# Optimization experiments

Hardware: AMD Instinct MI355X
Metric: run time of the kernel (lower is better)

Reference implementation:

```python
import jax, jax.numpy as jnp
import numpy as np

DIM = 384
HEADS = 12
HEAD_DIM = DIM // HEADS
WIN = (2, 7, 7)
NW_TOK = WIN[0] * WIN[1] * WIN[2]  # 98
SCALE = HEAD_DIM ** -0.5


def _relative_position_index():
    d = np.arange(WIN[0]); h = np.arange(WIN[1]); w = np.arange(WIN[2])
    coords = np.stack(np.meshgrid(d, h, w, indexing='ij'))  # [3,D,H,W]
    cf = coords.reshape(3, -1)  # [3, NW_TOK]
    rel = cf[:, :, None] - cf[:, None, :]  # [3, N, N]
    rel = rel.transpose(1, 2, 0).astype(np.int64)
    rel[:, :, 0] += WIN[0] - 1
    rel[:, :, 1] += WIN[1] - 1
    rel[:, :, 2] += WIN[2] - 1
    rel[:, :, 0] *= (2 * WIN[1] - 1) * (2 * WIN[2] - 1)
    rel[:, :, 1] *= 2 * WIN[2] - 1
    return rel.sum(-1)  # [NW_TOK, NW_TOK]


def setup_inputs() -> dict:
    key = jax.random.key(0)
    ks = jax.random.split(key, 6)
    B_, N = 1024, NW_TOK + 1
    nW = 64
    table_len = (2 * WIN[0] - 1) * (2 * WIN[1] - 1) * (2 * WIN[2] - 1)  # 507
    x = jax.random.normal(ks[0], (B_, N, DIM), dtype=jnp.float32)
    mask = jax.random.normal(ks[1], (nW, NW_TOK, NW_TOK), dtype=jnp.float32)
    W_qkv = jax.random.normal(ks[2], (DIM, 3 * DIM), dtype=jnp.float32) * 0.02
    rpb_table = jax.random.normal(ks[3], (table_len, HEADS), dtype=jnp.float32) * 0.02
    W_proj = jax.random.normal(ks[4], (DIM, DIM), dtype=jnp.float32) * 0.02
    b_proj = jnp.zeros((DIM,), dtype=jnp.float32)
    rpi = jnp.asarray(_relative_position_index(), dtype=jnp.int32)
    return {"x": x, "mask": mask, "W_qkv": W_qkv, "rpb_table": rpb_table,
            "W_proj": W_proj, "b_proj": b_proj, "rpi": rpi}


def reference(x, mask, W_qkv, rpb_table, W_proj, b_proj, rpi):
    B_, N, C = x.shape
    qkv = (x @ W_qkv).reshape(B_, N, 3, HEADS, HEAD_DIM)
    q, k, v = qkv[:, :, 0], qkv[:, :, 1], qkv[:, :, 2]  # [B_, N, H, hd]
    attn = jnp.einsum('bnhd,bmhd->bhnm', q * SCALE, k)  # [B_, H, N, N]
    # gathered relative position bias over non-class tokens, zero-padded for class token
    bias = rpb_table[rpi.reshape(-1)].reshape(NW_TOK, NW_TOK, HEADS).transpose(2, 0, 1)
    bias_full = jnp.pad(bias, ((0, 0), (1, 0), (1, 0)))  # [H, N, N]
    attn = attn + bias_full[None]
    nW = mask.shape[0]
    mask_full = jnp.pad(mask, ((0, 0), (1, 0), (1, 0)))  # [nW, N, N]
    attn = attn.reshape(B_ // nW, nW, HEADS, N, N) + mask_full[None, :, None]
    attn = attn.reshape(B_, HEADS, N, N)
    attn = jax.nn.softmax(attn, axis=-1)
    out = jnp.einsum('bhnm,bmhd->bnhd', attn, v).reshape(B_, N, C)
    out = out @ W_proj + b_proj
    return out[:, 1:], out[:, :1]
```

## Files before the change

### kernel.cpp

```cpp
#include <hip/hip_runtime.h>
#include <hip/hip_bf16.h>
#include <cstddef>
#include <cstdint>


using bf16 = __hip_bfloat16;
typedef short v8s __attribute__((ext_vector_type(8)));
typedef float v4f __attribute__((ext_vector_type(4)));

static constexpr int    NTOK   = 99;
static constexpr int    CDIM   = 384;
static constexpr int    NHEAD  = 12;
static constexpr int    NROWS  = 101376;
static constexpr size_t PLANE  = (size_t)NROWS * 32;
static constexpr float  SCALEF = 0.17677669529663687f;

__device__ __forceinline__ v4f mfma16x16x32(v8s a, v8s b, v4f c) {
  return __builtin_amdgcn_mfma_f32_16x16x32_bf16(a, b, c, 0, 0, 0);
}
__device__ __forceinline__ short f2bf(float f) {
  bf16 h = __float2bfloat16(f);
  return *reinterpret_cast<short*>(&h);
}

static constexpr size_t WT_QKV_OFF = 0;
static constexpr size_t WT_P_OFF   = 884736;
static constexpr size_t BIAS_OFF   = 884736 + 294912;
static constexpr size_t COMMON_END = 1650096;
static constexpr size_t O_WS_OFF   = COMMON_END;
static constexpr size_t WS_MID     = O_WS_OFF + (size_t)NROWS * 384 * 2;
static constexpr size_t BM_OFF     = COMMON_END;
static constexpr size_t QKV_OFF    = BM_OFF + (size_t)64 * NHEAD * NTOK * NTOK * 4;
static constexpr size_t WS_FULL    = QKV_OFF + (size_t)NROWS * 1152 * 2;

static constexpr int PREP_BASE = 1152 * 384 + 384 * 384 + NHEAD * 99 * 99;
static constexpr int PREP_BM   = 64 * NHEAD * 99 * 99;

__global__ void prep_kernel(const float* __restrict__ Wqkv, const float* __restrict__ Wproj,
                            const float* __restrict__ rpb,  const int* __restrict__ rpi,
                            const float* __restrict__ mask,
                            bf16* __restrict__ WtQKV, bf16* __restrict__ WtP,
                            float* __restrict__ BIAS, float* __restrict__ BM, int do_bm)
{
  int idx = blockIdx.x * 256 + threadIdx.x;
  if (idx < 1152 * 384) {
    int c = idx / 384, k = idx - c * 384;
    WtQKV[idx] = __float2bfloat16(Wqkv[k * 1152 + c]);
  } else if (idx < 1152 * 384 + 384 * 384) {
    int j = idx - 1152 * 384;
    int c = j / 384, k = j - c * 384;
    WtP[j] = __float2bfloat16(Wproj[k * 384 + c]);
  } else if (idx < PREP_BASE) {
    int j = idx - (1152 * 384 + 384 * 384);
    int h = j / (99 * 99), r = j - h * (99 * 99);
    int nn = r / 99, mm = r - nn * 99;
    float v = 0.f;
    if (nn > 0 && mm > 0) v = rpb[rpi[(nn - 1) * 98 + (mm - 1)] * NHEAD + h];
    BIAS[j] = v;
  } else if (do_bm && idx < PREP_BASE + PREP_BM) {
    int j = idx - PREP_BASE;
    int wi = j / (NHEAD * 9801);
    int r2 = j - wi * (NHEAD * 9801);
    int h = r2 / 9801, rr = r2 - h * 9801;
    int nn = rr / 99, mm = rr - nn * 99;
    float v = 0.f;
    if (nn > 0 && mm > 0)
      v = rpb[rpi[(nn - 1) * 98 + (mm - 1)] * NHEAD + h]
        + mask[((size_t)wi * 98 + (nn - 1)) * 98 + (mm - 1)];
    BM[j] = v;
  }
}

static constexpr int GQ_LD   = 72;
static constexpr int GQ_OFFB = 0;
static constexpr int GQ_OFFA = 192 * GQ_LD * 2;
static constexpr int GQ_LDS  = GQ_OFFA + 128 * GQ_LD * 2;

__global__ __launch_bounds__(512)
void k_qkv(const float* __restrict__ x, const bf16* __restrict__ WtQKV,
           bf16* __restrict__ qkv2)
{
  __shared__ __align__(16) char smem[GQ_LDS];
  bf16* B_lds = (bf16*)(smem + GQ_OFFB);
  bf16* A_lds = (bf16*)(smem + GQ_OFFA);

  const int tid  = threadIdx.x;
  const int wave = tid >> 6;
  const int lane = tid & 63;
  const int g    = lane >> 4;
  const int li   = lane & 15;
  const int tile = (blockIdx.x & 7) * 594 + (blockIdx.x >> 3);
  const int R0   = (tile / 6) * 128;
  const int CN   = (tile % 6) * 192;

  v4f acc[12];
  #pragma unroll
  for (int t = 0; t < 12; ++t) acc[t] = (v4f){0.f, 0.f, 0.f, 0.f};

  for (int kc = 0; kc < 6; ++kc) {
    const int k0 = kc * 64;
    #pragma unroll
    for (int p = 0; p < 3; ++p) {
      int it = tid + p * 512, rr = it >> 3, k8 = it & 7;
      *(v8s*)(B_lds + rr * GQ_LD + k8 * 8) =
          *(const v8s*)(WtQKV + (size_t)(CN + rr) * 384 + k0 + k8 * 8);
    }
    #pragma unroll
    for (int p = 0; p < 2; ++p) {
      int it = tid + p * 512, rr = it >> 3, k8 = it & 7;
      const float* src = x + (size_t)(R0 + rr) * 384 + k0 + k8 * 8;
      v4f x0 = *(const v4f*)(src);
      v4f x1 = *(const v4f*)(src + 4);
      v8s f;
      #pragma unroll
      for (int j = 0; j < 4; ++j) { f[j] = f2bf(x0[j]); f[j + 4] = f2bf(x1[j]); }
      *(v8s*)(A_lds + rr * GQ_LD + k8 * 8) = f;
    }
    __syncthreads();
    #pragma unroll
    for (int ks = 0; ks < 2; ++ks) {
      v8s ao = *(const v8s*)(A_lds + (16 * wave + li) * GQ_LD + ks * 32 + g * 8);
      #pragma unroll
      for (int t = 0; t < 12; ++t) {
        v8s bw = *(const v8s*)(B_lds + (16 * t + li) * GQ_LD + ks * 32 + g * 8);
        acc[t] = mfma16x16x32(ao, bw, acc[t]);
      }
    }
    __syncthreads();
  }

  const float scale = (CN < 384) ? SCALEF : 1.f;
  #pragma unroll
  for (int t = 0; t < 12; ++t) {
    int col = CN + 16 * t + li;
    int seg = col / 384, within = col - seg * 384;
    int hh = within >> 5, d = within & 31;
    bf16* plane = qkv2 + (size_t)(hh * 3 + seg) * PLANE;
    #pragma unroll
    for (int j = 0; j < 4; ++j) {
      int r = R0 + 16 * wave + g * 4 + j;
      plane[(size_t)r * 32 + d] = __float2bfloat16(acc[t][j] * scale);
    }
  }
}

static constexpr int A_QK_LD = 40;
static constexpr int A_VT_LD = 104;
static constexpr int A_P_LD  = 104;
static constexpr int A_OFF_Q = 0;
static constexpr int A_OFF_K = A_OFF_Q + 112 * A_QK_LD * 2;
static constexpr int A_OFF_V = A_OFF_K + 112 * A_QK_LD * 2;
static constexpr int A_OFF_P = A_OFF_V + 32  * A_VT_LD * 2;
static constexpr int A_LDS   = A_OFF_P + 112 * A_P_LD  * 2;

__global__ __launch_bounds__(448)
void k_attn(const float* __restrict__ BM, bf16* __restrict__ qkv2)
{
  __shared__ __align__(16) char smem[A_LDS];
  bf16* q_lds  = (bf16*)(smem + A_OFF_Q);
  bf16* k_lds  = (bf16*)(smem + A_OFF_K);
  bf16* vT_lds = (bf16*)(smem + A_OFF_V);
  bf16* P_lds  = (bf16*)(smem + A_OFF_P);

  const int b    = blockIdx.x;
  const int tid  = threadIdx.x;
  const int wave = tid >> 6;
  const int lane = tid & 63;
  const int g    = lane >> 4;
  const int li   = lane & 15;
  const int wi   = b & 63;

  const int r  = tid >> 2, l4 = tid & 3;
  const int rc = (r > 98) ? 98 : r;
  const size_t goff = ((size_t)b * NTOK + rc) * 32 + l4 * 8;

  {
    v8s pq = *(const v8s*)(qkv2 + 0 * PLANE + goff);
    v8s pk = *(const v8s*)(qkv2 + 1 * PLANE + goff);
    v8s pv = *(const v8s*)(qkv2 + 2 * PLANE + goff);
    *(v8s*)(q_lds + r * A_QK_LD + l4 * 8) = pq;
    *(v8s*)(k_lds + r * A_QK_LD + l4 * 8) = pk;
    if (r < NTOK) {
      #pragma unroll
      for (int e = 0; e < 8; ++e)
        *(short*)(vT_lds + (l4 * 8 + e) * A_VT_LD + r) = pv[e];
    }
  }
  __syncthreads();

  for (int h = 0; h < NHEAD; ++h) {
    v8s nq, nk, nv;
    if (h < NHEAD - 1) {
      nq = *(const v8s*)(qkv2 + (size_t)(h * 3 + 3) * PLANE + goff);
      nk = *(const v8s*)(qkv2 + (size_t)(h * 3 + 4) * PLANE + goff);
      nv = *(const v8s*)(qkv2 + (size_t)(h * 3 + 5) * PLANE + goff);
    }

    const float* bm = BM + (size_t)(wi * NHEAD + h) * 9801;
    float bmr[28];
    #pragma unroll
    for (int t = 0; t < 7; ++t) {
      int col = 16 * t + li; int colc = (col > 98) ? 98 : col;
      #pragma unroll
      for (int j = 0; j < 4; ++j) {
        int row = 16 * wave + g * 4 + j; int rowc = (row > 98) ? 98 : row;
        bmr[t * 4 + j] = bm[rowc * 99 + colc];
      }
    }

    v8s aq = *(const v8s*)(q_lds + (16 * wave + li) * A_QK_LD + g * 8);
    v4f sacc[7];
    #pragma unroll
    for (int t = 0; t < 7; ++t) {
      v8s bk = *(const v8s*)(k_lds + (16 * t + li) * A_QK_LD + g * 8);
      v4f z = (v4f){0.f, 0.f, 0.f, 0.f};
      sacc[t] = mfma16x16x32(aq, bk, z);
    }
    #pragma unroll
    for (int t = 0; t < 7; ++t) {
      int col = 16 * t + li;
      #pragma unroll
      for (int j = 0; j < 4; ++j) {
        float s = sacc[t][j];
        if (col >= NTOK) s = -1e30f;
        else             s += bmr[t * 4 + j];
        sacc[t][j] = s;
      }
    }
    float linv[4];
    #pragma unroll
    for (int j = 0; j < 4; ++j) {
      float m = -1e30f;
      #pragma unroll
      for (int t = 0; t < 7; ++t) m = fmaxf(m, sacc[t][j]);
      m = fmaxf(m, __shfl_xor(m, 1));
      m = fmaxf(m, __shfl_xor(m, 2));
      m = fmaxf(m, __shfl_xor(m, 4));
      m = fmaxf(m, __shfl_xor(m, 8));
      float l = 0.f;
      #pragma unroll
      for (int t = 0; t < 7; ++t) {
        float p = __expf(sacc[t][j] - m);
        sacc[t][j] = p;
        l += p;
      }
      l += __shfl_xor(l, 1);
      l += __shfl_xor(l, 2);
      l += __shfl_xor(l, 4);
      l += __shfl_xor(l, 8);
      linv[j] = 1.f / l;
      int row = 16 * wave + g * 4 + j;
      #pragma unroll
      for (int t = 0; t < 7; ++t) {
        int col = 16 * t + li;
        if (col < NTOK) P_lds[row * A_P_LD + col] = __float2bfloat16(sacc[t][j]);
      }
    }
    v4f oacc[2];
    oacc[0] = (v4f){0.f, 0.f, 0.f, 0.f};
    oacc[1] = (v4f){0.f, 0.f, 0.f, 0.f};
    #pragma unroll
    for (int ks = 0; ks < 3; ++ks) {
      v8s ap = *(const v8s*)(P_lds + (16 * wave + li) * A_P_LD + ks * 32 + g * 8);
      #pragma unroll
      for (int t = 0; t < 2; ++t) {
        v8s bv = *(const v8s*)(vT_lds + (16 * t + li) * A_VT_LD + ks * 32 + g * 8);
        oacc[t] = mfma16x16x32(ap, bv, oacc[t]);
      }
    }
    #pragma unroll
    for (int t = 0; t < 2; ++t) {
      float v0 = __bfloat162float(vT_lds[(16 * t + li) * A_VT_LD + 96]);
      float v1 = __bfloat162float(vT_lds[(16 * t + li) * A_VT_LD + 97]);
      float v2 = __bfloat162float(vT_lds[(16 * t + li) * A_VT_LD + 98]);
      #pragma unroll
      for (int j = 0; j < 4; ++j) {
        int row = 16 * wave + g * 4 + j;
        float p0 = __bfloat162float(P_lds[row * A_P_LD + 96]);
        float p1 = __bfloat162float(P_lds[row * A_P_LD + 97]);
        float p2 = __bfloat162float(P_lds[row * A_P_LD + 98]);
        oacc[t][j] += p0 * v0 + p1 * v1 + p2 * v2;
      }
    }
    bf16* oplane = qkv2 + (size_t)(h * 3) * PLANE;
    #pragma unroll
    for (int t = 0; t < 2; ++t) {
      #pragma unroll
      for (int j = 0; j < 4; ++j) {
        int row = 16 * wave + g * 4 + j;
        if (row < NTOK)
          oplane[((size_t)b * NTOK + row) * 32 + 16 * t + li] =
              __float2bfloat16(oacc[t][j] * linv[j]);
      }
    }
    __syncthreads();
    if (h < NHEAD - 1) {
      *(v8s*)(q_lds + r * A_QK_LD + l4 * 8) = nq;
      *(v8s*)(k_lds + r * A_QK_LD + l4 * 8) = nk;
      if (r < NTOK) {
        #pragma unroll
        for (int e = 0; e < 8; ++e)
          *(short*)(vT_lds + (l4 * 8 + e) * A_VT_LD + r) = nv[e];
      }
      __syncthreads();
    }
  }
}

static constexpr int K2_LD   = 72;
static constexpr int K2_OFFW = 0;
static constexpr int K2_OFFO = 192 * K2_LD * 2;
static constexpr int K2_LDS  = K2_OFFO + 128 * K2_LD * 2;

__global__ __launch_bounds__(512)
void k2_proj(const bf16* __restrict__ O_src, const int hm,
             const bf16* __restrict__ WtP, const float* __restrict__ bproj,
             float* __restrict__ out)
{
  __shared__ __align__(16) char smem[K2_LDS];
  bf16* W_lds = (bf16*)(smem + K2_OFFW);
  bf16* O_lds = (bf16*)(smem + K2_OFFO);

  const int tid  = threadIdx.x;
  const int wave = tid >> 6;
  const int lane = tid & 63;
  const int g    = lane >> 4;
  const int li   = lane & 15;
  const int tile = (blockIdx.x & 7) * 198 + (blockIdx.x >> 3);
  const int R0   = (tile >> 1) * 128;
  const int CN   = (tile & 1) * 192;

  v4f acc[12];
  #pragma unroll
  for (int t = 0; t < 12; ++t) acc[t] = (v4f){0.f, 0.f, 0.f, 0.f};

  for (int kc = 0; kc < 6; ++kc) {
    const int k0 = kc * 64;
    #pragma unroll
    for (int p = 0; p < 3; ++p) {
      int it = tid + p * 512, rr = it >> 3, k8 = it & 7;
      *(v8s*)(W_lds + rr * K2_LD + k8 * 8) =
          *(const v8s*)(WtP + (size_t)(CN + rr) * CDIM + k0 + k8 * 8);
    }
    #pragma unroll
    for (int p = 0; p < 2; ++p) {
      int it = tid + p * 512, rr = it >> 3, k8 = it & 7;
      const bf16* src;
      if (hm) {
        int c = k0 + k8 * 8, hh = c >> 5, d = c & 31;
        src = O_src + (size_t)(hh * 3) * PLANE + (size_t)(R0 + rr) * 32 + d;
      } else {
        src = O_src + (size_t)(R0 + rr) * 384 + k0 + k8 * 8;
      }
      *(v8s*)(O_lds + rr * K2_LD + k8 * 8) = *(const v8s*)src;
    }
    __syncthreads();
    #pragma unroll
    for (int ks = 0; ks < 2; ++ks) {
      v8s ao = *(const v8s*)(O_lds + (16 * wave + li) * K2_LD + ks * 32 + g * 8);
      #pragma unroll
      for (int t = 0; t < 12; ++t) {
        v8s bw = *(const v8s*)(W_lds + (16 * t + li) * K2_LD + ks * 32 + g * 8);
        acc[t] = mfma16x16x32(ao, bw, acc[t]);
      }
    }
    __syncthreads();
  }

  const size_t OUT2 = (size_t)1024 * 98 * CDIM;
  #pragma unroll
  for (int t = 0; t < 12; ++t) {
    int col = CN + 16 * t + li;
    float bb = bproj[col];
    #pragma unroll
    for (int j = 0; j < 4; ++j) {
      int rr = R0 + 16 * wave + g * 4 + j;
      int b = rr / 99, n = rr - b * 99;
      float v = acc[t][j] + bb;
      if (n == 0) out[OUT2 + (size_t)b * CDIM + col] = v;
      else        out[((size_t)b * 98 + (n - 1)) * CDIM + col] = v;
    }
  }
}

static constexpr int QK_LD = 40;
static constexpr int VT_LD = 136;
static constexpr int P_LD  = 136;
static constexpr int WS_LD = 104;
static constexpr int K1_OFF_Q = 0;
static constexpr int K1_OFF_K = K1_OFF_Q + 112 * QK_LD * 2;
static constexpr int K1_OFF_V = K1_OFF_K + 112 * QK_LD * 2;
static constexpr int K1_OFF_P = K1_OFF_V + 32  * VT_LD * 2;
static constexpr int K1_OFF_W = K1_OFF_P + 112 * P_LD  * 2;
static constexpr int K1_LDS   = K1_OFF_W + 96 * WS_LD * 2;

__global__ __launch_bounds__(512)
void k1_attn(const float* __restrict__ x, const float* __restrict__ mask,
             const float* __restrict__ BIAS, const bf16* __restrict__ WtQKV,
             bf16* __restrict__ O_ws)
{
  __shared__ __align__(16) char smem[K1_LDS];
  bf16* q_lds  = (bf16*)(smem + K1_OFF_Q);
  bf16* k_lds  = (bf16*)(smem + K1_OFF_K);
  bf16* vT_lds = (bf16*)(smem + K1_OFF_V);
  bf16* P_lds  = (bf16*)(smem + K1_OFF_P);
  bf16* w_lds  = (bf16*)(smem + K1_OFF_W);

  const int b    = blockIdx.x;
  const int tid  = threadIdx.x;
  const int wave = tid >> 6;
  const int lane = tid & 63;
  const int g    = lane >> 4;
  const int li   = lane & 15;
  const int wi   = b & 63;

  v8s afr[12];
  if (wave < 7) {
    int arow = 16 * wave + li; if (arow > 98) arow = 98;
    const float* xb = x + ((size_t)b * NTOK + arow) * CDIM + g * 8;
    #pragma unroll
    for (int s = 0; s < 12; ++s) {
      v4f x0 = *(const v4f*)(xb + s * 32);
      v4f x1 = *(const v4f*)(xb + s * 32 + 4);
      v8s f;
      #pragma unroll
      for (int j = 0; j < 4; ++j) { f[j] = f2bf(x0[j]); f[j + 4] = f2bf(x1[j]); }
      afr[s] = f;
    }
  }

  for (int h = 0; h < NHEAD; ++h) {
    v4f qacc[6];
    #pragma unroll
    for (int t = 0; t < 6; ++t) qacc[t] = (v4f){0.f, 0.f, 0.f, 0.f};
    #pragma unroll
    for (int c4 = 0; c4 < 4; ++c4) {
      for (int idx = tid; idx < 96 * 12; idx += 512) {
        int rr = idx / 12, ch = idx - rr * 12;
        int cg = (rr < 32) ? (h * 32 + rr)
               : (rr < 64) ? (CDIM + h * 32 + rr - 32)
                           : (2 * CDIM + h * 32 + rr - 64);
        *(v8s*)(w_lds + rr * WS_LD + ch * 8) =
            *(const v8s*)(WtQKV + (size_t)cg * CDIM + c4 * 96 + ch * 8);
      }
      __syncthreads();
      if (wave < 7) {
        #pragma unroll
        for (int ss = 0; ss < 3; ++ss) {
          const int s = c4 * 3 + ss;
          #pragma unroll
          for (int t = 0; t < 6; ++t) {
            v8s bw = *(const v8s*)(w_lds + (16 * t + li) * WS_LD + ss * 32 + g * 8);
            qacc[t] = mfma16x16x32(afr[s], bw, qacc[t]);
          }
        }
      }
      __syncthreads();
    }
    if (wave < 7) {
      #pragma unroll
      for (int t = 0; t < 6; ++t) {
        #pragma unroll
        for (int j = 0; j < 4; ++j) {
          int row = 16 * wave + g * 4 + j;
          int col = 16 * (t & 1) + li;
          float v = qacc[t][j];
          if (t < 2)      q_lds[row * QK_LD + col] = __float2bfloat16(v * SCALEF);
          else if (t < 4) k_lds[row * QK_LD + col] = __float2bfloat16(v);
          else            vT_lds[col * VT_LD + row] = __float2bfloat16(v);
        }
      }
    }
    vT_lds[(tid >> 4) * VT_LD + 112 + (tid & 15)] = __float2bfloat16(0.f);
    __syncthreads();

    if (wave < 7) {
      v8s aq = *(const v8s*)(q_lds + (16 * wave + li) * QK_LD + g * 8);
      v4f sacc[7];
      #pragma unroll
      for (int t = 0; t < 7; ++t) {
        v8s bk = *(const v8s*)(k_lds + (16 * t + li) * QK_LD + g * 8);
        v4f z = (v4f){0.f, 0.f, 0.f, 0.f};
        sacc[t] = mfma16x16x32(aq, bk, z);
      }
      #pragma unroll
      for (int t = 0; t < 7; ++t) {
        int col = 16 * t + li;
        #pragma unroll
        for (int j = 0; j < 4; ++j) {
          int row = 16 * wave + g * 4 + j;
          float s = sacc[t][j];
          if (col >= NTOK) s = -1e30f;
          else if (row < NTOK) {
            s += BIAS[(h * NTOK + row) * NTOK + col];
            if (row > 0 && col > 0)
              s += mask[((size_t)wi * 98 + (row - 1)) * 98 + (col - 1)];
          }
          sacc[t][j] = s;
        }
      }
      float linv[4];
      #pragma unroll
      for (int j = 0; j < 4; ++j) {
        float m = -1e30f;
        #pragma unroll
        for (int t = 0; t < 7; ++t) m = fmaxf(m, sacc[t][j]);
        m = fmaxf(m, __shfl_xor(m, 1));
        m = fmaxf(m, __shfl_xor(m, 2));
        m = fmaxf(m, __shfl_xor(m, 4));
        m = fmaxf(m, __shfl_xor(m, 8));
        float l = 0.f;
        #pragma unroll
        for (int t = 0; t < 7; ++t) {
          float p = __expf(sacc[t][j] - m);
          sacc[t][j] = p;
          l += p;
        }
        l += __shfl_xor(l, 1);
        l += __shfl_xor(l, 2);
        l += __shfl_xor(l, 4);
        l += __shfl_xor(l, 8);
        linv[j] = 1.f / l;
        int row = 16 * wave + g * 4 + j;
        #pragma unroll
        for (int t = 0; t < 7; ++t)
          P_lds[row * P_LD + 16 * t + li] = __float2bfloat16(sacc[t][j]);
        P_lds[row * P_LD + 112 + li] = __float2bfloat16(0.f);
      }
      v4f oacc[2];
      oacc[0] = (v4f){0.f, 0.f, 0.f, 0.f};
      oacc[1] = (v4f){0.f, 0.f, 0.f, 0.f};
      #pragma unroll
      for (int ks = 0; ks < 4; ++ks) {
        v8s ap = *(const v8s*)(P_lds + (16 * wave + li) * P_LD + ks * 32 + g * 8);
        #pragma unroll
        for (int t = 0; t < 2; ++t) {
          v8s bv = *(const v8s*)(vT_lds + (16 * t + li) * VT_LD + ks * 32 + g * 8);
          oacc[t] = mfma16x16x32(ap, bv, oacc[t]);
        }
      }
      #pragma unroll
      for (int t = 0; t < 2; ++t) {
        #pragma unroll
        for (int j = 0; j < 4; ++j) {
          int row = 16 * wave + g * 4 + j;
          if (row < NTOK)
            O_ws[((size_t)b * 99 + row) * CDIM + h * 32 + 16 * t + li] =
                __float2bfloat16(oacc[t][j] * linv[j]);
        }
      }
    }
    __syncthreads();
  }
}

static constexpr int M_O_LD = 392;
static constexpr int M_OFF_O = 0;
static constexpr int M_OFF_Q = M_OFF_O + 99  * M_O_LD * 2;
static constexpr int M_OFF_K = M_OFF_Q + 112 * QK_LD * 2;
static constexpr int M_OFF_V = M_OFF_K + 112 * QK_LD * 2;
static constexpr int M_OFF_P = M_OFF_V + 32  * VT_LD * 2;
static constexpr int M_OFF_W = M_OFF_P + 112 * P_LD  * 2;
static constexpr int M_LDS   = M_OFF_W + 96 * WS_LD * 2;

__global__ __launch_bounds__(512)
void fused_mono(const float* __restrict__ x, const float* __restrict__ mask,
                const float* __restrict__ bproj, const float* __restrict__ BIAS,
                const bf16* __restrict__ WtQKV, const bf16* __restrict__ WtP,
                float* __restrict__ out)
{
  __shared__ __align__(16) char smem[M_LDS];
  bf16* O_lds  = (bf16*)(smem + M_OFF_O);
  bf16* q_lds  = (bf16*)(smem + M_OFF_Q);
  bf16* k_lds  = (bf16*)(smem + M_OFF_K);
  bf16* vT_lds = (bf16*)(smem + M_OFF_V);
  bf16* P_lds  = (bf16*)(smem + M_OFF_P);
  bf16* w_lds  = (bf16*)(smem + M_OFF_W);

  const int b    = blockIdx.x;
  const int tid  = threadIdx.x;
  const int wave = tid >> 6;
  const int lane = tid & 63;
  const int g    = lane >> 4;
  const int li   = lane & 15;
  const int wi   = b & 63;

  v8s afr[12];
  if (wave < 7) {
    int arow = 16 * wave + li; if (arow > 98) arow = 98;
    const float* xb = x + ((size_t)b * NTOK + arow) * CDIM + g * 8;
    #pragma unroll
    for (int s = 0; s < 12; ++s) {
      v4f x0 = *(const v4f*)(xb + s * 32);
      v4f x1 = *(const v4f*)(xb + s * 32 + 4);
      v8s f;
      #pragma unroll
      for (int j = 0; j < 4; ++j) { f[j] = f2bf(x0[j]); f[j + 4] = f2bf(x1[j]); }
      afr[s] = f;
    }
  }

  for (int h = 0; h < NHEAD; ++h) {
    v4f qacc[6];
    #pragma unroll
    for (int t = 0; t < 6; ++t) qacc[t] = (v4f){0.f, 0.f, 0.f, 0.f};
    #pragma unroll
    for (int c4 = 0; c4 < 4; ++c4) {
      for (int idx = tid; idx < 96 * 12; idx += 512) {
        int rr = idx / 12, ch = idx - rr * 12;
        int cg = (rr < 32) ? (h * 32 + rr)
               : (rr < 64) ? (CDIM + h * 32 + rr - 32)
                           : (2 * CDIM + h * 32 + rr - 64);
        *(v8s*)(w_lds + rr * WS_LD + ch * 8) =
            *(const v8s*)(WtQKV + (size_t)cg * CDIM + c4 * 96 + ch * 8);
      }
      __syncthreads();
      if (wave < 7) {
        #pragma unroll
        for (int ss = 0; ss < 3; ++ss) {
          const int s = c4 * 3 + ss;
          #pragma unroll
          for (int t = 0; t < 6; ++t) {
            v8s bw = *(const v8s*)(w_lds + (16 * t + li) * WS_LD + ss * 32 + g * 8);
            qacc[t] = mfma16x16x32(afr[s], bw, qacc[t]);
          }
        }
      }
      __syncthreads();
    }
    if (wave < 7) {
      #pragma unroll
      for (int t = 0; t < 6; ++t) {
        #pragma unroll
        for (int j = 0; j < 4; ++j) {
          int row = 16 * wave + g * 4 + j;
          int col = 16 * (t & 1) + li;
          float v = qacc[t][j];
          if (t < 2)      q_lds[row * QK_LD + col] = __float2bfloat16(v * SCALEF);
          else if (t < 4) k_lds[row * QK_LD + col] = __float2bfloat16(v);
          else            vT_lds[col * VT_LD + row] = __float2bfloat16(v);
        }
      }
    }
    vT_lds[(tid >> 4) * VT_LD + 112 + (tid & 15)] = __float2bfloat16(0.f);
    __syncthreads();

    if (wave < 7) {
      v8s aq = *(const v8s*)(q_lds + (16 * wave + li) * QK_LD + g * 8);
      v4f sacc[7];
      #pragma unroll
      for (int t = 0; t < 7; ++t) {
        v8s bk = *(const v8s*)(k_lds + (16 * t + li) * QK_LD + g * 8);
        v4f z = (v4f){0.f, 0.f, 0.f, 0.f};
        sacc[t] = mfma16x16x32(aq, bk, z);
      }
      #pragma unroll
      for (int t = 0; t < 7; ++t) {
        int col = 16 * t + li;
        #pragma unroll
        for (int j = 0; j < 4; ++j) {
          int row = 16 * wave + g * 4 + j;
          float s = sacc[t][j];
          if (col >= NTOK) s = -1e30f;
          else if (row < NTOK) {
            s += BIAS[(h * NTOK + row) * NTOK + col];
            if (row > 0 && col > 0)
              s += mask[((size_t)wi * 98 + (row - 1)) * 98 + (col - 1)];
          }
          sacc[t][j] = s;
        }
      }
      float linv[4];
      #pragma unroll
      for (int j = 0; j < 4; ++j) {
        float m = -1e30f;
        #pragma unroll
        for (int t = 0; t < 7; ++t) m = fmaxf(m, sacc[t][j]);
        m = fmaxf(m, __shfl_xor(m, 1));
        m = fmaxf(m, __shfl_xor(m, 2));
        m = fmaxf(m, __shfl_xor(m, 4));
        m = fmaxf(m, __shfl_xor(m, 8));
        float l = 0.f;
        #pragma unroll
        for (int t = 0; t < 7; ++t) {
          float p = __expf(sacc[t][j] - m);
          sacc[t][j] = p;
          l += p;
        }
        l += __shfl_xor(l, 1);
        l += __shfl_xor(l, 2);
        l += __shfl_xor(l, 4);
        l += __shfl_xor(l, 8);
        linv[j] = 1.f / l;
        int row = 16 * wave + g * 4 + j;
        #pragma unroll
        for (int t = 0; t < 7; ++t)
          P_lds[row * P_LD + 16 * t + li] = __float2bfloat16(sacc[t][j]);
        P_lds[row * P_LD + 112 + li] = __float2bfloat16(0.f);
      }
      v4f oacc[2];
      oacc[0] = (v4f){0.f, 0.f, 0.f, 0.f};
      oacc[1] = (v4f){0.f, 0.f, 0.f, 0.f};
      #pragma unroll
      for (int ks = 0; ks < 4; ++ks) {
        v8s ap = *(const v8s*)(P_lds + (16 * wave + li) * P_LD + ks * 32 + g * 8);
        #pragma unroll
        for (int t = 0; t < 2; ++t) {
          v8s bv = *(const v8s*)(vT_lds + (16 * t + li) * VT_LD + ks * 32 + g * 8);
          oacc[t] = mfma16x16x32(ap, bv, oacc[t]);
        }
      }
      #pragma unroll
      for (int t = 0; t < 2; ++t) {
        #pragma unroll
        for (int j = 0; j < 4; ++j) {
          int row = 16 * wave + g * 4 + j;
          if (row < NTOK)
            O_lds[row * M_O_LD + h * 32 + 16 * t + li] =
                __float2bfloat16(oacc[t][j] * linv[j]);
        }
      }
    }
    __syncthreads();
  }

  const size_t OUT2 = (size_t)1024 * 98 * CDIM;
  const int orow_clamped = (16 * wave + li > 98) ? 98 : 16 * wave + li;
  for (int cc = 0; cc < 4; ++cc) {
    v4f pacc[6];
    #pragma unroll
    for (int t = 0; t < 6; ++t) pacc[t] = (v4f){0.f, 0.f, 0.f, 0.f};
    for (int c4 = 0; c4 < 4; ++c4) {
      for (int idx = tid; idx < 96 * 12; idx += 512) {
        int rr = idx / 12, ch = idx - rr * 12;
        *(v8s*)(w_lds + rr * WS_LD + ch * 8) =
            *(const v8s*)(WtP + ((size_t)(cc * 96 + rr)) * CDIM + c4 * 96 + ch * 8);
      }
      __syncthreads();
      if (wave < 7) {
        #pragma unroll
        for (int ss = 0; ss < 3; ++ss) {
          const int s = c4 * 3 + ss;
          v8s ao = *(const v8s*)(O_lds + orow_clamped * M_O_LD + s * 32 + g * 8);
          #pragma unroll
          for (int t = 0; t < 6; ++t) {
            v8s bw = *(const v8s*)(w_lds + (16 * t + li) * WS_LD + ss * 32 + g * 8);
            pacc[t] = mfma16x16x32(ao, bw, pacc[t]);
          }
        }
      }
      __syncthreads();
    }
    if (wave < 7) {
      #pragma unroll
      for (int t = 0; t < 6; ++t) {
        #pragma unroll
        for (int j = 0; j < 4; ++j) {
          int row = 16 * wave + g * 4 + j;
          if (row < NTOK) {
            int col = cc * 96 + 16 * t + li;
            float v = pacc[t][j] + bproj[col];
            if (row == 0) out[OUT2 + (size_t)b * CDIM + col] = v;
            else          out[((size_t)b * 98 + (row - 1)) * CDIM + col] = v;
          }
        }
      }
    }
  }
}

extern "C" void kernel_launch(void* const* d_in, const int* in_sizes, int n_in,
                              void* d_out, int out_size, void* d_ws, size_t ws_size,
                              hipStream_t stream) {
  const float* x     = (const float*)d_in[0];
  const float* mask  = (const float*)d_in[1];
  const float* Wqkv  = (const float*)d_in[2];
  const float* rpb   = (const float*)d_in[3];
  const float* Wproj = (const float*)d_in[4];
  const float* bproj = (const float*)d_in[5];
  const int*   rpi   = (const int*)d_in[6];

  bf16*  WtQKV = (bf16*)((char*)d_ws + WT_QKV_OFF);
  bf16*  WtP   = (bf16*)((char*)d_ws + WT_P_OFF);
  float* BIAS  = (float*)((char*)d_ws + BIAS_OFF);

  const bool full = (ws_size >= WS_FULL);
  const int prep_items = full ? (PREP_BASE + PREP_BM) : PREP_BASE;
  float* BM = (float*)((char*)d_ws + BM_OFF);
  prep_kernel<<<(prep_items + 255) / 256, 256, 0, stream>>>(
      Wqkv, Wproj, rpb, rpi, mask, WtQKV, WtP, BIAS, BM, full ? 1 : 0);

  if (full) {
    bf16* qkv2 = (bf16*)((char*)d_ws + QKV_OFF);
    k_qkv<<<792 * 6, 512, 0, stream>>>(x, WtQKV, qkv2);
    k_attn<<<1024, 448, 0, stream>>>(BM, qkv2);
    k2_proj<<<792 * 2, 512, 0, stream>>>(qkv2, 1, WtP, bproj, (float*)d_out);
  } else if (ws_size >= WS_MID) {
    bf16* O_ws = (bf16*)((char*)d_ws + O_WS_OFF);
    k1_attn<<<1024, 512, 0, stream>>>(x, mask, BIAS, WtQKV, O_ws);
    k2_proj<<<792 * 2, 512, 0, stream>>>(O_ws, 0, WtP, bproj, (float*)d_out);
  } else {
    fused_mono<<<1024, 512, 0, stream>>>(x, mask, bproj, BIAS, WtQKV, WtP,
                                         (float*)d_out);
  }
}
```

Baseline: 446.8 us.

## Use 2x4 wave tiling in GEMMs, stage QKV stores, split attention heads

Both GEMM kernels move from giving each wave a 16-row strip across all 192 columns to a 2x4 wave grid with 64x48 sub-tiles. This cuts redundant LDS fragment reads per MFMA. The QKV epilogue now stages bf16 results through shared memory so each thread writes 16-byte vectors into the head-major planes instead of scattered 2-byte stores. The attention kernel is split across a second grid dimension of two 6-head groups to double the block count for more parallelism, at the cost of extra epilogue barriers and reusing GEMM LDS for staging.

```diff
diff --git a/kernel.cpp b/kernel.cpp
--- a/kernel.cpp
+++ b/kernel.cpp
@@ -71,10 +71,11 @@
   }
 }
 
-static constexpr int GQ_LD   = 72;
-static constexpr int GQ_OFFB = 0;
-static constexpr int GQ_OFFA = 192 * GQ_LD * 2;
-static constexpr int GQ_LDS  = GQ_OFFA + 128 * GQ_LD * 2;
+static constexpr int GQ_LD    = 72;
+static constexpr int GQ_OFFB  = 0;
+static constexpr int GQ_OFFA  = 192 * GQ_LD * 2;
+static constexpr int GQ_LDS   = GQ_OFFA + 128 * GQ_LD * 2;
+static constexpr int CSTG_LD  = 104;
 
 __global__ __launch_bounds__(512)
 void k_qkv(const float* __restrict__ x, const bf16* __restrict__ WtQKV,
@@ -83,9 +84,12 @@
   __shared__ __align__(16) char smem[GQ_LDS];
   bf16* B_lds = (bf16*)(smem + GQ_OFFB);
   bf16* A_lds = (bf16*)(smem + GQ_OFFA);
+  bf16* C_stg = (bf16*)(smem);
 
   const int tid  = threadIdx.x;
   const int wave = tid >> 6;
+  const int wm   = wave >> 2;
+  const int wn   = wave & 3;
   const int lane = tid & 63;
   const int g    = lane >> 4;
   const int li   = lane & 15;
@@ -93,9 +97,11 @@
   const int R0   = (tile / 6) * 128;
   const int CN   = (tile % 6) * 192;
 
-  v4f acc[12];
+  v4f acc[4][3];
   #pragma unroll
-  for (int t = 0; t < 12; ++t) acc[t] = (v4f){0.f, 0.f, 0.f, 0.f};
+  for (int mi = 0; mi < 4; ++mi)
+    #pragma unroll
+    for (int ni = 0; ni < 3; ++ni) acc[mi][ni] = (v4f){0.f, 0.f, 0.f, 0.f};
 
   for (int kc = 0; kc < 6; ++kc) {
     const int k0 = kc * 64;
@@ -119,27 +125,45 @@
     __syncthreads();
     #pragma unroll
     for (int ks = 0; ks < 2; ++ks) {
-      v8s ao = *(const v8s*)(A_lds + (16 * wave + li) * GQ_LD + ks * 32 + g * 8);
-      #pragma unroll
-      for (int t = 0; t < 12; ++t) {
-        v8s bw = *(const v8s*)(B_lds + (16 * t + li) * GQ_LD + ks * 32 + g * 8);
-        acc[t] = mfma16x16x32(ao, bw, acc[t]);
-      }
+      v8s af[4], bfr[3];
+      #pragma unroll
+      for (int mi = 0; mi < 4; ++mi)
+        af[mi] = *(const v8s*)(A_lds + (wm * 64 + mi * 16 + li) * GQ_LD + ks * 32 + g * 8);
+      #pragma unroll
+      for (int ni = 0; ni < 3; ++ni)
+        bfr[ni] = *(const v8s*)(B_lds + (wn * 48 + ni * 16 + li) * GQ_LD + ks * 32 + g * 8);
+      #pragma unroll
+      for (int mi = 0; mi < 4; ++mi)
+        #pragma unroll
+        for (int ni = 0; ni < 3; ++ni)
+          acc[mi][ni] = mfma16x16x32(af[mi], bfr[ni], acc[mi][ni]);
     }
     __syncthreads();
   }
 
   const float scale = (CN < 384) ? SCALEF : 1.f;
+  const int r_ep = tid >> 2, d8 = tid & 3;
   #pragma unroll
-  for (int t = 0; t < 12; ++t) {
-    int col = CN + 16 * t + li;
-    int seg = col / 384, within = col - seg * 384;
-    int hh = within >> 5, d = within & 31;
-    bf16* plane = qkv2 + (size_t)(hh * 3 + seg) * PLANE;
-    #pragma unroll
-    for (int j = 0; j < 4; ++j) {
-      int r = R0 + 16 * wave + g * 4 + j;
-      plane[(size_t)r * 32 + d] = __float2bfloat16(acc[t][j] * scale);
+  for (int half = 0; half < 2; ++half) {
+    __syncthreads();
+    if ((wn >> 1) == half) {
+      #pragma unroll
+      for (int mi = 0; mi < 4; ++mi)
+        #pragma unroll
+        for (int ni = 0; ni < 3; ++ni)
+          #pragma unroll
+          for (int j = 0; j < 4; ++j)
+            C_stg[(wm * 64 + mi * 16 + g * 4 + j) * CSTG_LD + (wn & 1) * 48 + ni * 16 + li] =
+                __float2bfloat16(acc[mi][ni][j] * scale);
+    }
+    __syncthreads();
+    #pragma unroll
+    for (int cidx = 0; cidx < 3; ++cidx) {
+      int c_global = CN + half * 96 + cidx * 32;
+      int seg = c_global / 384, hh = (c_global % 384) >> 5;
+      bf16* plane = qkv2 + (size_t)(hh * 3 + seg) * PLANE;
+      v8s val = *(const v8s*)(C_stg + r_ep * CSTG_LD + cidx * 32 + d8 * 8);
+      *(v8s*)(plane + (size_t)(R0 + r_ep) * 32 + d8 * 8) = val;
     }
   }
 }
@@ -163,6 +187,7 @@
   bf16* P_lds  = (bf16*)(smem + A_OFF_P);
 
   const int b    = blockIdx.x;
+  const int h0   = blockIdx.y * 6;
   const int tid  = threadIdx.x;
   const int wave = tid >> 6;
   const int lane = tid & 63;
@@ -175,9 +200,9 @@
   const size_t goff = ((size_t)b * NTOK + rc) * 32 + l4 * 8;
 
   {
-    v8s pq = *(const v8s*)(qkv2 + 0 * PLANE + goff);
-    v8s pk = *(const v8s*)(qkv2 + 1 * PLANE + goff);
-    v8s pv = *(const v8s*)(qkv2 + 2 * PLANE + goff);
+    v8s pq = *(const v8s*)(qkv2 + (size_t)(h0 * 3 + 0) * PLANE + goff);
+    v8s pk = *(const v8s*)(qkv2 + (size_t)(h0 * 3 + 1) * PLANE + goff);
+    v8s pv = *(const v8s*)(qkv2 + (size_t)(h0 * 3 + 2) * PLANE + goff);
     *(v8s*)(q_lds + r * A_QK_LD + l4 * 8) = pq;
     *(v8s*)(k_lds + r * A_QK_LD + l4 * 8) = pk;
     if (r < NTOK) {
@@ -188,9 +213,10 @@
   }
   __syncthreads();
 
-  for (int h = 0; h < NHEAD; ++h) {
+  for (int hi = 0; hi < 6; ++hi) {
+    const int h = h0 + hi;
     v8s nq, nk, nv;
-    if (h < NHEAD - 1) {
+    if (hi < 5) {
       nq = *(const v8s*)(qkv2 + (size_t)(h * 3 + 3) * PLANE + goff);
       nk = *(const v8s*)(qkv2 + (size_t)(h * 3 + 4) * PLANE + goff);
       nv = *(const v8s*)(qkv2 + (size_t)(h * 3 + 5) * PLANE + goff);
@@ -294,7 +320,7 @@
       }
     }
     __syncthreads();
-    if (h < NHEAD - 1) {
+    if (hi < 5) {
       *(v8s*)(q_lds + r * A_QK_LD + l4 * 8) = nq;
       *(v8s*)(k_lds + r * A_QK_LD + l4 * 8) = nk;
       if (r < NTOK) {
@@ -323,6 +349,8 @@
 
   const int tid  = threadIdx.x;
   const int wave = tid >> 6;
+  const int wm   = wave >> 2;
+  const int wn   = wave & 3;
   const int lane = tid & 63;
   const int g    = lane >> 4;
   const int li   = lane & 15;
@@ -330,9 +358,11 @@
   const int R0   = (tile >> 1) * 128;
   const int CN   = (tile & 1) * 192;
 
-  v4f acc[12];
+  v4f acc[4][3];
   #pragma unroll
-  for (int t = 0; t < 12; ++t) acc[t] = (v4f){0.f, 0.f, 0.f, 0.f};
+  for (int mi = 0; mi < 4; ++mi)
+    #pragma unroll
+    for (int ni = 0; ni < 3; ++ni) acc[mi][ni] = (v4f){0.f, 0.f, 0.f, 0.f};
 
   for (int kc = 0; kc < 6; ++kc) {
     const int k0 = kc * 64;
@@ -357,30 +387,38 @@
     __syncthreads();
     #pragma unroll
     for (int ks = 0; ks < 2; ++ks) {
-      v8s ao = *(const v8s*)(O_lds + (16 * wave + li) * K2_LD + ks * 32 + g * 8);
-      #pragma unroll
-      for (int t = 0; t < 12; ++t) {
-        v8s bw = *(const v8s*)(W_lds + (16 * t + li) * K2_LD + ks * 32 + g * 8);
-        acc[t] = mfma16x16x32(ao, bw, acc[t]);
-      }
+      v8s af[4], bfr[3];
+      #pragma unroll
+      for (int mi = 0; mi < 4; ++mi)
+        af[mi] = *(const v8s*)(O_lds + (wm * 64 + mi * 16 + li) * K2_LD + ks * 32 + g * 8);
+      #pragma unroll
+      for (int ni = 0; ni < 3; ++ni)
+        bfr[ni] = *(const v8s*)(W_lds + (wn * 48 + ni * 16 + li) * K2_LD + ks * 32 + g * 8);
+      #pragma unroll
+      for (int mi = 0; mi < 4; ++mi)
+        #pragma unroll
+        for (int ni = 0; ni < 3; ++ni)
+          acc[mi][ni] = mfma16x16x32(af[mi], bfr[ni], acc[mi][ni]);
     }
     __syncthreads();
   }
 
   const size_t OUT2 = (size_t)1024 * 98 * CDIM;
   #pragma unroll
-  for (int t = 0; t < 12; ++t) {
-    int col = CN + 16 * t + li;
-    float bb = bproj[col];
-    #pragma unroll
-    for (int j = 0; j < 4; ++j) {
-      int rr = R0 + 16 * wave + g * 4 + j;
-      int b = rr / 99, n = rr - b * 99;
-      float v = acc[t][j] + bb;
-      if (n == 0) out[OUT2 + (size_t)b * CDIM + col] = v;
-      else        out[((size_t)b * 98 + (n - 1)) * CDIM + col] = v;
-    }
-  }
+  for (int mi = 0; mi < 4; ++mi)
+    #pragma unroll
+    for (int ni = 0; ni < 3; ++ni) {
+      int col = CN + wn * 48 + ni * 16 + li;
+      float bb = bproj[col];
+      #pragma unroll
+      for (int j = 0; j < 4; ++j) {
+        int rr = R0 + wm * 64 + mi * 16 + g * 4 + j;
+        int b = rr / 99, n = rr - b * 99;
+        float v = acc[mi][ni][j] + bb;
+        if (n == 0) out[OUT2 + (size_t)b * CDIM + col] = v;
+        else        out[((size_t)b * 98 + (n - 1)) * CDIM + col] = v;
+      }
+    }
 }
 
 static constexpr int QK_LD = 40;
@@ -793,7 +831,7 @@
   if (full) {
     bf16* qkv2 = (bf16*)((char*)d_ws + QKV_OFF);
     k_qkv<<<792 * 6, 512, 0, stream>>>(x, WtQKV, qkv2);
-    k_attn<<<1024, 448, 0, stream>>>(BM, qkv2);
+    k_attn<<<dim3(1024, 2), 448, 0, stream>>>(BM, qkv2);
     k2_proj<<<792 * 2, 512, 0, stream>>>(qkv2, 1, WtP, bproj, (float*)d_out);
   } else if (ws_size >= WS_MID) {
     bf16* O_ws = (bf16*)((char*)d_ws + O_WS_OFF);
```

After: 425.7 us. 4.7% less time.
